# Performance work log

Hardware: AMD Instinct MI355X
Metric: run time of the kernel (lower is better)

## Reference

```python
import jax, jax.numpy as jnp
import numpy as np

N = 1_048_576   # number of time samples (light-curve length)
M = 8           # number of quasisep Exp kernel terms (state dimension)
LOG2PI = float(np.log(2.0 * np.pi))


def setup_inputs() -> dict:
    key = jax.random.key(0)
    k1, k2, k3, k4, k5 = jax.random.split(key, 5)
    # unsorted-but-nearly-sorted timestamps; module argsorts internally
    t = jax.random.uniform(k1, (N,), dtype=jnp.float32) * (N / 10.0)
    y = jax.random.normal(k2, (N,), dtype=jnp.float32)
    yerr = 0.1 + 0.05 * jax.random.uniform(k3, (N,), dtype=jnp.float32)
    # interleaved [log_scale_j, log_sigma_j] for M Exp terms, as ravel_pytree would produce
    log_scale = jnp.log(10.0) + 0.5 * jax.random.normal(k4, (M,), dtype=jnp.float32)
    log_sigma = 0.3 * jax.random.normal(k5, (M,), dtype=jnp.float32)
    log_kernel_param = jnp.stack([log_scale, log_sigma], axis=1).reshape(-1)
    return {"t": t, "y": y, "yerr": yerr, "log_kernel_param": log_kernel_param}


def _kalman_log_prob(ts, ys, diag, scale, sigma):
    """GP log-likelihood for k(tau)=sum_j sigma_j^2 exp(-tau/scale_j) via Kalman filter.

    State: M independent OU components; observation h = ones(M); zero mean.
    """
    Pinf = sigma * sigma                                   # stationary variances [M]
    dt = jnp.concatenate([jnp.zeros((1,), ts.dtype), jnp.diff(ts)])  # [N]

    def step(carry, inp):
        m, P, ll = carry                                   # m:[M], P:[M,M]
        dtn, yn, dn = inp
        phi = jnp.exp(-dtn / scale)                        # transition diag [M]
        m_pred = phi * m
        # P_pred = Phi P Phi^T + Q,  Q = diag(Pinf*(1-phi^2))
        P_pred = (phi[:, None] * phi[None, :]) * P + jnp.diag(Pinf * (1.0 - phi * phi))
        Ph = P_pred.sum(axis=1)                            # P_pred @ h
        S = Ph.sum() + dn                                  # innovation variance
        v = yn - m_pred.sum()                              # innovation (zero mean)
        K = Ph / S                                         # Kalman gain
        m_new = m_pred + K * v
        P_new = P_pred - K[:, None] * Ph[None, :]
        ll_new = ll - 0.5 * (LOG2PI + jnp.log(S) + v * v / S)
        return (m_new, P_new, ll_new), None

    m0 = jnp.zeros((M,), ts.dtype)
    P0 = jnp.diag(Pinf)
    (_, _, ll), _ = jax.lax.scan(step, (m0, P0, jnp.zeros((), ts.dtype)), (dt, ys, diag))
    return ll


def reference(t, y, yerr, log_kernel_param):
    # UniVarModel.log_prob: sort by time, diag = yerr^2 (has_jitter=False),
    # kernel params exponentiated, zero mean.
    inds = jnp.argsort(t)
    ts, ys, diag = t[inds], y[inds], yerr[inds] ** 2
    p = jnp.exp(log_kernel_param)
    scale, sigma = p[0::2], p[1::2]
    return _kalman_log_prob(ts, ys, diag, scale, sigma)
```

## Files before the change

### kernel.cpp

```cpp
#include <hip/hip_runtime.h>
#include <stdint.h>

typedef unsigned long long u64;

#define CHUNK 64
#define WARM  8
#define SLEN  (WARM + CHUNK)
#define CPW   8
#define PD    8
#define NB    16384
#define NR    1024
#define BCAP  128
#define RCAP  2048
#define HBLK  64
#define LOG2PI_F 1.8378770664093453f

__device__ __forceinline__ int bucket_of(float tv, float scale) {
    int b = (int)(tv * scale);
    return b > (NB - 1) ? (NB - 1) : (b < 0 ? 0 : b);
}

__global__ __launch_bounds__(256) void hist_k(const float4* __restrict__ t4,
                                              unsigned* __restrict__ hp,
                                              float scale, int n4) {
    __shared__ unsigned lh[NR];
    for (int v = threadIdx.x; v < NR; v += 256) lh[v] = 0u;
    __syncthreads();
    for (int i = blockIdx.x * 256 + threadIdx.x; i < n4; i += gridDim.x * 256) {
        float4 tv = t4[i];
        atomicAdd(&lh[bucket_of(tv.x, scale) >> 4], 1u);
        atomicAdd(&lh[bucket_of(tv.y, scale) >> 4], 1u);
        atomicAdd(&lh[bucket_of(tv.z, scale) >> 4], 1u);
        atomicAdd(&lh[bucket_of(tv.w, scale) >> 4], 1u);
    }
    __syncthreads();
    for (int v = threadIdx.x; v < NR; v += 256)
        hp[blockIdx.x * NR + v] = lh[v];
}

__global__ __launch_bounds__(1024) void scan_k(const unsigned* __restrict__ hp,
                                               unsigned* __restrict__ roff,
                                               unsigned* __restrict__ rcnt) {
    __shared__ unsigned ws[16];
    const int r = threadIdx.x;
    unsigned tot = 0;
#pragma unroll 8
    for (int b = 0; b < HBLK; ++b) tot += hp[b * NR + r];
    unsigned s = tot;
#pragma unroll
    for (int d = 1; d < 64; d <<= 1) {
        unsigned v = __shfl_up(s, d);
        if ((r & 63) >= d) s += v;
    }
    if ((r & 63) == 63) ws[r >> 6] = s;
    __syncthreads();
    if (r < 16) {
        unsigned v = ws[r];
#pragma unroll
        for (int d = 1; d < 16; d <<= 1) {
            unsigned x = __shfl_up(v, d);
            if (r >= d) v += x;
        }
        ws[r] = v;
    }
    __syncthreads();
    unsigned wbase = (r >= 64) ? ws[(r >> 6) - 1] : 0u;
    unsigned excl = wbase + s - tot;
    roff[r] = excl; rcnt[r] = excl;
    if (r == NR - 1) roff[NR] = excl + tot;
}

__global__ __launch_bounds__(1024) void scatter1(const float4* __restrict__ t4,
                                                 const float4* __restrict__ y4,
                                                 const float4* __restrict__ e4,
                                                 const unsigned* __restrict__ roff,
                                                 unsigned* __restrict__ rcnt,
                                                 u64* __restrict__ keys1,
                                                 float2* __restrict__ pay1,
                                                 float scale) {
    __shared__ unsigned lh[NR], rb[NR], rloc[NR];
    const int tid = threadIdx.x;
    lh[tid] = 0u;
    __syncthreads();
    const int i0 = blockIdx.x * 2048 + tid;
    float4 a = t4[i0], b = t4[i0 + 1024];
    float4 ya = y4[i0], yb = y4[i0 + 1024];
    float4 ea = e4[i0], eb = e4[i0 + 1024];
    float tv[8] = {a.x, a.y, a.z, a.w, b.x, b.y, b.z, b.w};
    float yv[8] = {ya.x, ya.y, ya.z, ya.w, yb.x, yb.y, yb.z, yb.w};
    float ev[8] = {ea.x, ea.y, ea.z, ea.w, eb.x, eb.y, eb.z, eb.w};
    unsigned id0 = 4u * (unsigned)i0, id1 = 4u * (unsigned)(i0 + 1024);
    unsigned ids[8] = {id0, id0 + 1, id0 + 2, id0 + 3,
                       id1, id1 + 1, id1 + 2, id1 + 3};
    int rr[8]; unsigned lp[8];
#pragma unroll
    for (int k = 0; k < 8; ++k) {
        rr[k] = bucket_of(tv[k], scale) >> 4;
        lp[k] = atomicAdd(&lh[rr[k]], 1u);
    }
    __syncthreads();
    {
        unsigned c = lh[tid];
        unsigned base = c ? atomicAdd(&rcnt[tid], c) : 0u;
        rb[tid] = base;
        rloc[tid] = base - roff[tid];
    }
    __syncthreads();
#pragma unroll
    for (int k = 0; k < 8; ++k) {
        unsigned bits = __float_as_uint(tv[k]);
        unsigned mk = (bits & 0x80000000u) ? ~bits : (bits | 0x80000000u);
        unsigned pos = rb[rr[k]] + lp[k];
        unsigned slot = (rloc[rr[k]] + lp[k]) & 0x7FFu;
        keys1[pos] = ((u64)mk << 32) | ((u64)(ids[k] << 11)) | (u64)slot;
        pay1[pos] = make_float2(yv[k], ev[k] * ev[k]);
    }
}

__device__ __forceinline__ float decode_key(unsigned h) {
    unsigned b = (h & 0x80000000u) ? (h ^ 0x80000000u) : ~h;
    return __uint_as_float(b);
}

__global__ __launch_bounds__(256) void sort_k(const u64* __restrict__ keys1,
                                              const float2* __restrict__ pay1,
                                              const unsigned* __restrict__ roff,
                                              float* __restrict__ tS,
                                              float* __restrict__ ysA,
                                              float* __restrict__ dgA,
                                              float scale) {
    __shared__ u64 sk[16 * BCAP];
    __shared__ float2 sp[RCAP];
    __shared__ unsigned lh[16], pre[16];
    const int r = blockIdx.x;
    const int tid = threadIdx.x;
    for (int v = tid; v < 16 * BCAP; v += 256) sk[v] = ~0ull;
    if (tid < 16) lh[tid] = 0u;
    __syncthreads();
    const unsigned s = roff[r], e = roff[r + 1];
    for (unsigned u = s + tid; u < e; u += 256) {
        if (u - s < (unsigned)RCAP) sp[u - s] = pay1[u];
        u64 kk = keys1[u];
        int b16 = bucket_of(decode_key((unsigned)(kk >> 32)), scale) & 15;
        unsigned lp = atomicAdd(&lh[b16], 1u);
        if (lp < (unsigned)BCAP) sk[b16 * BCAP + lp] = kk;
    }
    __syncthreads();
    if (tid == 0) {
        unsigned acc = 0;
#pragma unroll
        for (int c = 0; c < 16; ++c) {
            pre[c] = acc;
            unsigned cc = lh[c];
            acc += (cc > (unsigned)BCAP) ? (unsigned)BCAP : cc;
        }
    }
    for (int k = 2; k <= BCAP; k <<= 1) {
        for (int j = k >> 1; j >= 1; j >>= 1) {
#pragma unroll
            for (int it = 0; it < 4; ++it) {
                int w = it * 256 + tid;
                int q = w >> 6, p = w & 63;
                int i = ((p & ~(j - 1)) << 1) | (p & (j - 1));
                int si = q * BCAP + i, sp_ = si + j;
                bool up = ((i & k) == 0);
                u64 a = sk[si], bb = sk[sp_];
                if ((a > bb) == up) { sk[si] = bb; sk[sp_] = a; }
            }
            __syncthreads();
        }
    }
#pragma unroll
    for (int cp = 0; cp < 8; ++cp) {
        int c = cp * 2 + (tid >> 7);
        int el = tid & 127;
        unsigned cc = lh[c]; cc = (cc > (unsigned)BCAP) ? (unsigned)BCAP : cc;
        if (el < (int)cc) {
            u64 kk = sk[c * BCAP + el];
            unsigned pos = s + pre[c] + el;
            float2 yd = sp[(unsigned)(kk & 0x7FFull)];
            tS[pos] = decode_key((unsigned)(kk >> 32));
            ysA[pos] = yd.x;
            dgA[pos] = yd.y;
        }
    }
}

#define DPPMOV(x, ctrl) __int_as_float(__builtin_amdgcn_update_dpp( \
        0, __float_as_int(x), (ctrl), 0xF, 0xF, true))
#define GSUM8(s, x) { s = (x) + DPPMOV((x), 0xB1); s += DPPMOV(s, 0x4E); s += DPPMOV(s, 0x141); }
#define GATHER8(v, x) { \
    v[0] = (x); v[1] = DPPMOV((x), 0xB1); v[2] = DPPMOV((x), 0x4E); \
    v[3] = DPPMOV(v[1], 0x4E); v[7] = DPPMOV((x), 0x141); \
    v[6] = DPPMOV(v[1], 0x141); v[5] = DPPMOV(v[2], 0x141); v[4] = DPPMOV(v[3], 0x141); }

__global__ __launch_bounds__(64) void kalman8(
    const float* __restrict__ tS, const float* __restrict__ ysA,
    const float* __restrict__ dgA, const float* __restrict__ lkp,
    float* __restrict__ llp) {
    __shared__ float4 sty[SLEN * 8];
    const int lane = threadIdx.x & 63;
    const int g = lane >> 3, l = lane & 7;
    const int bi = blockIdx.x;
    const long base = (long)bi * (CPW * CHUNK) - WARM;

    const float INF = __builtin_huge_valf();
    const float t0 = tS[0];
#pragma unroll
    for (int gg = 0; gg < CPW; ++gg) {
        for (int v = lane; v < SLEN; v += 64) {
            long gi = base + gg * CHUNK + v;
            float tv, yv, dv;
            if (gi >= 0) { tv = tS[gi]; yv = ysA[gi]; dv = dgA[gi]; }
            else { tv = t0; yv = 0.0f; dv = INF; }
            sty[v * 8 + ((gg + v) & 7)] = make_float4(tv, yv, dv, 0.0f);
        }
    }
    long gp = base + g * CHUNK - 1;
    float stp = (gp >= 0) ? tS[gp] : t0;
    __syncthreads();

    const float L2E = 1.44269504088896340736f;
    const float LN2 = 0.6931471805599453f;
    const float c_own = -L2E * __expf(-lkp[2 * l]);
    const float Pinf  = __expf(2.0f * lkp[2 * l + 1]);

    float P[8];
    P[0] = Pinf;
#pragma unroll
    for (int k = 1; k < 8; ++k) P[k] = 0.0f;
    float m = 0.0f, llog = 0.0f, lvw = 0.0f;

#define KSTEP(LS, SCORED) { \
    const int slot_ = (LS) * 8 + ((g + (LS)) & 7); \
    float4 q4 = sty[slot_]; \
    float dtc = q4.x - stp; stp = q4.x; float yc = q4.y; float dc = q4.z; \
    float phi = __builtin_amdgcn_exp2f(dtc * c_own); \
    float fv[8]; GATHER8(fv, phi) \
    float q0 = phi * phi; \
    float dadd = fmaf(-q0, Pinf, Pinf); \
    float Pp[8]; \
    Pp[0] = fmaf(q0, P[0], dadd); \
    _Pragma("unroll") \
    for (int k = 1; k < 8; ++k) Pp[k] = (phi * fv[k]) * P[k]; \
    float Ph = ((Pp[0] + Pp[1]) + (Pp[2] + Pp[3])) + ((Pp[4] + Pp[5]) + (Pp[6] + Pp[7])); \
    float mp = phi * m; \
    float Ss; GSUM8(Ss, Ph) \
    float ms; GSUM8(ms, mp) \
    float S = Ss + dc; \
    float v = yc - ms; \
    float invS = __builtin_amdgcn_rcpf(S); \
    float w = v * invS; \
    float K = Ph * invS; \
    float pv[8]; GATHER8(pv, Ph) \
    _Pragma("unroll") \
    for (int k = 0; k < 8; ++k) P[k] = fmaf(-K, pv[k], Pp[k]); \
    m = fmaf(Ph, w, mp); \
    if (SCORED) { llog += __builtin_amdgcn_logf(S); lvw = fmaf(v, w, lvw); } }

    for (int ls = 0; ls < WARM; ls += PD) {
#pragma unroll
        for (int u = 0; u < PD; ++u) KSTEP(ls + u, false)
    }
    for (int ls = WARM; ls < SLEN; ls += PD) {
#pragma unroll
        for (int u = 0; u < PD; ++u) KSTEP(ls + u, true)
    }
#undef KSTEP

    if (l == 0)
        llp[bi * CPW + g] = -0.5f * (CHUNK * LOG2PI_F + LN2 * llog + lvw);
}

__global__ __launch_bounds__(256) void reduce_ll(const float* __restrict__ llp,
                                                 float* __restrict__ out, int g) {
    __shared__ float sred[4];
    int tid = threadIdx.x;
    float s = 0.0f;
    for (int i = tid; i < g; i += 256) s += llp[i];
    for (int m = 1; m < 64; m <<= 1) s += __shfl_xor(s, m);
    if ((tid & 63) == 0) sred[tid >> 6] = s;
    __syncthreads();
    if (tid == 0) out[0] = sred[0] + sred[1] + sred[2] + sred[3];
}

extern "C" void kernel_launch(void* const* d_in, const int* in_sizes, int n_in,
                              void* d_out, int out_size, void* d_ws, size_t ws_size,
                              hipStream_t stream) {
    const float* t    = (const float*)d_in[0];
    const float* y    = (const float*)d_in[1];
    const float* yerr = (const float*)d_in[2];
    const float* lkp  = (const float*)d_in[3];
    float* out = (float*)d_out;
    const int n = in_sizes[0];

    u64*      keys1 = (u64*)d_ws;
    float2*   pay1  = (float2*)((char*)d_ws + (size_t)n * 8);
    float*    tS    = (float*)((char*)d_ws + (size_t)n * 16);
    float*    ysA   = (float*)((char*)d_ws + (size_t)n * 20);
    float*    dgA   = (float*)((char*)d_ws + (size_t)n * 24);
    float*    llp   = (float*)((char*)d_ws + (size_t)n * 28);
    unsigned* hp    = (unsigned*)(llp + 16384);
    unsigned* roff  = hp + HBLK * NR;
    unsigned* rcnt  = roff + NR + 64;

    const float scale = (float)NB / ((float)n / 10.0f);
    const int n4 = n / 4;

    hist_k<<<HBLK, 256, 0, stream>>>((const float4*)t, hp, scale, n4);
    scan_k<<<1, 1024, 0, stream>>>(hp, roff, rcnt);
    scatter1<<<n4 / 2048, 1024, 0, stream>>>((const float4*)t, (const float4*)y,
                                             (const float4*)yerr, roff, rcnt,
                                             keys1, pay1, scale);
    sort_k<<<NR, 256, 0, stream>>>(keys1, pay1, roff, tS, ysA, dgA, scale);

    const int G = n / CHUNK;
    kalman8<<<G / CPW, 64, 0, stream>>>(tS, ysA, dgA, lkp, llp);
    reduce_ll<<<1, 256, 0, stream>>>(llp, out, G);
}
```

Baseline: 106.0 us.

## Pack sorted t/y/diag into float4 array and halve Kalman chunk size

```diff
diff --git a/kernel.cpp b/kernel.cpp
--- a/kernel.cpp
+++ b/kernel.cpp
@@ -3,7 +3,7 @@
 
 typedef unsigned long long u64;
 
-#define CHUNK 64
+#define CHUNK 32
 #define WARM  8
 #define SLEN  (WARM + CHUNK)
 #define CPW   8
@@ -125,9 +125,7 @@
 __global__ __launch_bounds__(256) void sort_k(const u64* __restrict__ keys1,
                                               const float2* __restrict__ pay1,
                                               const unsigned* __restrict__ roff,
-                                              float* __restrict__ tS,
-                                              float* __restrict__ ysA,
-                                              float* __restrict__ dgA,
+                                              float4* __restrict__ tyd,
                                               float scale) {
     __shared__ u64 sk[16 * BCAP];
     __shared__ float2 sp[RCAP];
@@ -179,9 +177,7 @@
             u64 kk = sk[c * BCAP + el];
             unsigned pos = s + pre[c] + el;
             float2 yd = sp[(unsigned)(kk & 0x7FFull)];
-            tS[pos] = decode_key((unsigned)(kk >> 32));
-            ysA[pos] = yd.x;
-            dgA[pos] = yd.y;
+            tyd[pos] = make_float4(decode_key((unsigned)(kk >> 32)), yd.x, yd.y, 0.0f);
         }
     }
 }
@@ -195,8 +191,7 @@
     v[6] = DPPMOV(v[1], 0x141); v[5] = DPPMOV(v[2], 0x141); v[4] = DPPMOV(v[3], 0x141); }
 
 __global__ __launch_bounds__(64) void kalman8(
-    const float* __restrict__ tS, const float* __restrict__ ysA,
-    const float* __restrict__ dgA, const float* __restrict__ lkp,
+    const float4* __restrict__ tyd, const float* __restrict__ lkp,
     float* __restrict__ llp) {
     __shared__ float4 sty[SLEN * 8];
     const int lane = threadIdx.x & 63;
@@ -205,19 +200,15 @@
     const long base = (long)bi * (CPW * CHUNK) - WARM;
 
     const float INF = __builtin_huge_valf();
-    const float t0 = tS[0];
-#pragma unroll
-    for (int gg = 0; gg < CPW; ++gg) {
-        for (int v = lane; v < SLEN; v += 64) {
-            long gi = base + gg * CHUNK + v;
-            float tv, yv, dv;
-            if (gi >= 0) { tv = tS[gi]; yv = ysA[gi]; dv = dgA[gi]; }
-            else { tv = t0; yv = 0.0f; dv = INF; }
-            sty[v * 8 + ((gg + v) & 7)] = make_float4(tv, yv, dv, 0.0f);
-        }
+    const float4 e0 = tyd[0];
+    for (int p = lane; p < CPW * SLEN; p += 64) {
+        int gg = p / SLEN, v = p - gg * SLEN;
+        long gi = base + gg * CHUNK + v;
+        float4 f = (gi >= 0) ? tyd[gi] : make_float4(e0.x, 0.0f, INF, 0.0f);
+        sty[v * 8 + ((gg + v) & 7)] = f;
     }
     long gp = base + g * CHUNK - 1;
-    float stp = (gp >= 0) ? tS[gp] : t0;
+    float stp = (gp >= 0) ? tyd[gp].x : e0.x;
     __syncthreads();
 
     const float L2E = 1.44269504088896340736f;
@@ -296,11 +287,9 @@
 
     u64*      keys1 = (u64*)d_ws;
     float2*   pay1  = (float2*)((char*)d_ws + (size_t)n * 8);
-    float*    tS    = (float*)((char*)d_ws + (size_t)n * 16);
-    float*    ysA   = (float*)((char*)d_ws + (size_t)n * 20);
-    float*    dgA   = (float*)((char*)d_ws + (size_t)n * 24);
-    float*    llp   = (float*)((char*)d_ws + (size_t)n * 28);
-    unsigned* hp    = (unsigned*)(llp + 16384);
+    float4*   tyd   = (float4*)((char*)d_ws + (size_t)n * 16);
+    float*    llp   = (float*)((char*)d_ws + (size_t)n * 32);
+    unsigned* hp    = (unsigned*)(llp + 32768);
     unsigned* roff  = hp + HBLK * NR;
     unsigned* rcnt  = roff + NR + 64;
 
@@ -312,9 +301,9 @@
     scatter1<<<n4 / 2048, 1024, 0, stream>>>((const float4*)t, (const float4*)y,
                                              (const float4*)yerr, roff, rcnt,
                                              keys1, pay1, scale);
-    sort_k<<<NR, 256, 0, stream>>>(keys1, pay1, roff, tS, ysA, dgA, scale);
+    sort_k<<<NR, 256, 0, stream>>>(keys1, pay1, roff, tyd, scale);
 
     const int G = n / CHUNK;
-    kalman8<<<G / CPW, 64, 0, stream>>>(tS, ysA, dgA, lkp, llp);
+    kalman8<<<G / CPW, 64, 0, stream>>>(tyd, lkp, llp);
     reduce_ll<<<1, 256, 0, stream>>>(llp, out, G);
 }
```

Result: slower. 121.0 us (+14.1%).
